# Performance work log

Hardware: AMD Instinct MI355X
Metric: run time of the kernel (lower is better)

Reference implementation:

```python
import jax, jax.numpy as jnp
import numpy as np

EPS = float(np.finfo(np.float32).eps)

# (joint_id, joint_name, parent_name) in the module's fkm_computation_order
ORDER = [
    (1, 'rHip', 'hip'), (2, 'rKnee', 'rHip'), (3, 'rAnkle', 'rKnee'), (4, 'rToe', 'rAnkle'),
    (6, 'lHip', 'hip'), (7, 'lKnee', 'lHip'), (8, 'lAnkle', 'lKnee'), (9, 'lToe', 'lAnkle'),
    (11, 'spine', 'hip'), (12, 'spine1', 'spine'), (13, 'thorax', 'spine1'), (14, 'neck', 'thorax'),
    (15, 'head', 'neck'), (16, 'lShoulderAnchor', 'spine1'), (17, 'lShoulder', 'lShoulderAnchor'),
    (18, 'lElbow', 'lShoulder'), (19, 'lWrist', 'lElbow'), (20, 'lThumb', 'lWrist'),
    (22, 'lWristEnd', 'lWrist'), (24, 'rShoulderAnchor', 'spine1'), (25, 'rShoulder', 'rShoulderAnchor'),
    (26, 'rElbow', 'rShoulder'), (27, 'rWrist', 'rElbow'), (28, 'rThumb', 'rWrist'),
    (30, 'rWristEnd', 'rWrist'),
]


def axis_angle_to_matrix(a):
    """Rodrigues formula, batched. a: [B,3] -> [B,3,3]."""
    theta = jnp.linalg.norm(a, axis=-1, keepdims=True)  # [B,1]
    r = a / (theta + EPS)                               # [B,3]
    r0, r1, r2 = r[:, 0], r[:, 1], r[:, 2]
    z = jnp.zeros_like(r0)
    # skew-symmetric S with S[0,1]=-r2, S[0,2]=r1, S[1,2]=-r0 (as in torch code)
    S = jnp.stack([
        jnp.stack([z, -r2, r1], axis=-1),
        jnp.stack([r2, z, -r0], axis=-1),
        jnp.stack([-r1, r0, z], axis=-1),
    ], axis=-2)  # [B,3,3]
    th = theta[..., None]  # [B,1,1]
    I = jnp.eye(3, dtype=a.dtype)
    return I + jnp.sin(th) * S + (1.0 - jnp.cos(th)) * (S @ S)


def setup_inputs() -> dict:
    key = jax.random.key(0)
    k1, k2 = jax.random.split(key)
    B = 262144
    x = jax.random.normal(k1, (B, 99), dtype=jnp.float32)
    offset = jax.random.normal(k2, (32, 3), dtype=jnp.float32)
    return {"x": x, "offset": offset}


def reference(x, offset):
    # hip root: position from first 3 dims, orientation from dims 3:6
    pos = {"hip": offset[0] + x[:, 0:3]}                # [B,3]
    ang = {"hip": axis_angle_to_matrix(x[:, 3:6])}      # [B,3,3]
    # local rotations for every joint in the chain: dims [3*id+3 : 3*id+6]
    local = {name: axis_angle_to_matrix(x[:, 3 * i + 3: 3 * i + 6]) for i, name, _ in ORDER}
    # sequential forward kinematics down the tree
    for i, cur, par in ORDER:
        # offset[i] @ R_parent  (row-vector times matrix), then translate
        pos[cur] = jnp.einsum('j,bjk->bk', offset[i], ang[par]) + pos[par]
        ang[cur] = local[cur] @ ang[par]
    # positions in the same order as get_joint_positions(): hip then chain order
    return jnp.stack([pos['hip']] + [pos[c] for _, c, _ in ORDER], axis=1)  # [B,26,3]
```

## Files before the change

### kernel.cpp

```cpp
#include <hip/hip_runtime.h>

#define ROWS 64
#define TPB  192
#define XDIM 99
#define NJ   26
#define OUTW 78

__device__ __forceinline__ float fast_rcp(float a)  { return __builtin_amdgcn_rcpf(a); }
__device__ __forceinline__ float fast_sqrt(float a) { return __builtin_amdgcn_sqrtf(a); }

__device__ __forceinline__ void rodrigues(float ax, float ay, float az, float* R) {
    const float EPS = 1.1920928955078125e-07f;
    float t = fast_sqrt(ax*ax + ay*ay + az*az);
    float inv = fast_rcp(t + EPS);
    float r0 = ax*inv, r1 = ay*inv, r2 = az*inv;
    float s = __sinf(t);
    float c = __cosf(t);
    float omc = 1.0f - c;
    float r00 = r0*r0, r11 = r1*r1, r22 = r2*r2;
    float r01 = r0*r1, r02 = r0*r2, r12 = r1*r2;
    R[0] = 1.0f - omc*(r11 + r22);
    R[1] = -s*r2 + omc*r01;
    R[2] =  s*r1 + omc*r02;
    R[3] =  s*r2 + omc*r01;
    R[4] = 1.0f - omc*(r00 + r22);
    R[5] = -s*r0 + omc*r12;
    R[6] = -s*r1 + omc*r02;
    R[7] =  s*r0 + omc*r12;
    R[8] = 1.0f - omc*(r00 + r11);
}

__global__ __launch_bounds__(TPB, 8) void skel_fk(const float* __restrict__ x,
                                                  const float* __restrict__ off,
                                                  float* __restrict__ out) {
    __shared__ float buf[ROWS * XDIM];
    const int t = threadIdx.x;
    const int w = t >> 6;
    const int l = t & 63;
    const int row0 = blockIdx.x * ROWS;

    {
        const float* gsrc = x + (long long)row0 * XDIM;
        const float* gw = gsrc + w * 2112 + l * 4;
        float* lw = buf + w * 2112;
        #pragma unroll
        for (int j = 0; j < 8; ++j) {
            __builtin_amdgcn_global_load_lds(
                (const __attribute__((address_space(1))) unsigned int*)(gw + j * 256),
                (__attribute__((address_space(3))) unsigned int*)(lw + j * 256),
                16, 0, 0);
        }
        __builtin_amdgcn_global_load_lds(
            (const __attribute__((address_space(1))) unsigned int*)(gsrc + w * 2112 + 2048 + l),
            (__attribute__((address_space(3))) unsigned int*)(buf + w * 2112 + 2048),
            4, 0, 0);
    }
    __syncthreads();

    const int r = l;
    const int k = w;
    float* wrow = &buf[r * XDIM];
    const float* row = wrow;

    constexpr int OFF_IDX[NJ] = {0,1,2,3,4,6,7,8,9,11,12,13,14,15,16,17,18,19,20,22,24,25,26,27,28,30};
    constexpr int PAR[NJ]     = {-1,0,1,2,3,0,5,6,7,0,9,10,11,12,10,14,15,16,17,17,10,20,21,22,23,23};

    float ac[NJ][3];
    float pp[NJ];

    {
        float R[9];
        rodrigues(row[3], row[4], row[5], R);
        ac[0][0] = (k == 0) ? R[0] : ((k == 1) ? R[1] : R[2]);
        ac[0][1] = (k == 0) ? R[3] : ((k == 1) ? R[4] : R[5]);
        ac[0][2] = (k == 0) ? R[6] : ((k == 1) ? R[7] : R[8]);
        pp[0] = off[k] + row[k];
    }

    #pragma unroll
    for (int s = 1; s < NJ; ++s) {
        const int i  = OFF_IDX[s];
        const int pa = PAR[s];
        float L[9];
        rodrigues(row[3*i+3], row[3*i+4], row[3*i+5], L);
        const float o0 = off[3*i], o1 = off[3*i+1], o2 = off[3*i+2];
        pp[s] = o0*ac[pa][0] + o1*ac[pa][1] + o2*ac[pa][2] + pp[pa];
        ac[s][0] = L[0]*ac[pa][0] + L[1]*ac[pa][1] + L[2]*ac[pa][2];
        ac[s][1] = L[3]*ac[pa][0] + L[4]*ac[pa][1] + L[5]*ac[pa][2];
        ac[s][2] = L[6]*ac[pa][0] + L[7]*ac[pa][1] + L[8]*ac[pa][2];
    }

    __syncthreads();

    #pragma unroll
    for (int s = 0; s < NJ; ++s)
        wrow[3*s + k] = pp[s];
    __syncthreads();

    {
        float* oblk = out + (long long)row0 * OUTW;
        #pragma unroll
        for (int j = 0; j < 26; ++j) {
            int m = t + j * TPB;
            int rr = m / OUTW;
            int cc = m - rr * OUTW;
            oblk[m] = buf[rr * XDIM + cc];
        }
    }
}

extern "C" void kernel_launch(void* const* d_in, const int* in_sizes, int n_in,
                              void* d_out, int out_size, void* d_ws, size_t ws_size,
                              hipStream_t stream) {
    const float* x   = (const float*)d_in[0];
    const float* off = (const float*)d_in[1];
    float* out = (float*)d_out;
    const int B = in_sizes[0] / XDIM;
    const int grid = B / ROWS;
    skel_fk<<<grid, TPB, 0, stream>>>(x, off, out);
}
```

Baseline: 40.11 us.

## Process two row slabs per block with both loads issued up front

Each block now handles two 64-row slabs. It issues the global-to-LDS loads for both slabs before the first barrier, then computes and writes each slab in turn. The barriers become lightweight lgkmcnt waits, sin and cos are fused into one sincos call, and launch bounds drop to 4 waves per SIMD. The aim is to amortize block launch and barrier overhead and to overlap the second slab's load with work. The cost is double the LDS per block, which halves occupancy.

```diff
diff --git a/kernel.cpp b/kernel.cpp
--- a/kernel.cpp
+++ b/kernel.cpp
@@ -1,10 +1,14 @@
 #include <hip/hip_runtime.h>
 
 #define ROWS 64
+#define NSLAB 2
 #define TPB  192
 #define XDIM 99
 #define NJ   26
 #define OUTW 78
+#define SLABF (ROWS * XDIM)
+
+#define LGKM_BAR() asm volatile("s_waitcnt lgkmcnt(0)\n\ts_barrier" ::: "memory")
 
 __device__ __forceinline__ float fast_rcp(float a)  { return __builtin_amdgcn_rcpf(a); }
 __device__ __forceinline__ float fast_sqrt(float a) { return __builtin_amdgcn_sqrtf(a); }
@@ -14,8 +18,8 @@
     float t = fast_sqrt(ax*ax + ay*ay + az*az);
     float inv = fast_rcp(t + EPS);
     float r0 = ax*inv, r1 = ay*inv, r2 = az*inv;
-    float s = __sinf(t);
-    float c = __cosf(t);
+    float s, c;
+    __sincosf(t, &s, &c);
     float omc = 1.0f - c;
     float r00 = r0*r0, r11 = r1*r1, r22 = r2*r2;
     float r01 = r0*r1, r02 = r0*r2, r12 = r1*r2;
@@ -30,19 +34,20 @@
     R[8] = 1.0f - omc*(r00 + r11);
 }
 
-__global__ __launch_bounds__(TPB, 8) void skel_fk(const float* __restrict__ x,
+__global__ __launch_bounds__(TPB, 4) void skel_fk(const float* __restrict__ x,
                                                   const float* __restrict__ off,
                                                   float* __restrict__ out) {
-    __shared__ float buf[ROWS * XDIM];
+    __shared__ float buf[NSLAB][SLABF];
     const int t = threadIdx.x;
     const int w = t >> 6;
     const int l = t & 63;
-    const int row0 = blockIdx.x * ROWS;
+    const int row0 = blockIdx.x * (ROWS * NSLAB);
 
-    {
-        const float* gsrc = x + (long long)row0 * XDIM;
-        const float* gw = gsrc + w * 2112 + l * 4;
-        float* lw = buf + w * 2112;
+    #pragma unroll
+    for (int sl = 0; sl < NSLAB; ++sl) {
+        const float* gs = x + (long long)(row0 + sl * ROWS) * XDIM;
+        const float* gw = gs + w * 2112 + l * 4;
+        float* lw = &buf[sl][0] + w * 2112;
         #pragma unroll
         for (int j = 0; j < 8; ++j) {
             __builtin_amdgcn_global_load_lds(
@@ -51,60 +56,63 @@
                 16, 0, 0);
         }
         __builtin_amdgcn_global_load_lds(
-            (const __attribute__((address_space(1))) unsigned int*)(gsrc + w * 2112 + 2048 + l),
-            (__attribute__((address_space(3))) unsigned int*)(buf + w * 2112 + 2048),
+            (const __attribute__((address_space(1))) unsigned int*)(gs + w * 2112 + 2048 + l),
+            (__attribute__((address_space(3))) unsigned int*)(&buf[sl][0] + w * 2112 + 2048),
             4, 0, 0);
     }
     __syncthreads();
 
-    const int r = l;
-    const int k = w;
-    float* wrow = &buf[r * XDIM];
-    const float* row = wrow;
-
     constexpr int OFF_IDX[NJ] = {0,1,2,3,4,6,7,8,9,11,12,13,14,15,16,17,18,19,20,22,24,25,26,27,28,30};
     constexpr int PAR[NJ]     = {-1,0,1,2,3,0,5,6,7,0,9,10,11,12,10,14,15,16,17,17,10,20,21,22,23,23};
 
-    float ac[NJ][3];
-    float pp[NJ];
-
-    {
-        float R[9];
-        rodrigues(row[3], row[4], row[5], R);
-        ac[0][0] = (k == 0) ? R[0] : ((k == 1) ? R[1] : R[2]);
-        ac[0][1] = (k == 0) ? R[3] : ((k == 1) ? R[4] : R[5]);
-        ac[0][2] = (k == 0) ? R[6] : ((k == 1) ? R[7] : R[8]);
-        pp[0] = off[k] + row[k];
-    }
+    const int k = w;
 
     #pragma unroll
-    for (int s = 1; s < NJ; ++s) {
-        const int i  = OFF_IDX[s];
-        const int pa = PAR[s];
-        float L[9];
-        rodrigues(row[3*i+3], row[3*i+4], row[3*i+5], L);
-        const float o0 = off[3*i], o1 = off[3*i+1], o2 = off[3*i+2];
-        pp[s] = o0*ac[pa][0] + o1*ac[pa][1] + o2*ac[pa][2] + pp[pa];
-        ac[s][0] = L[0]*ac[pa][0] + L[1]*ac[pa][1] + L[2]*ac[pa][2];
-        ac[s][1] = L[3]*ac[pa][0] + L[4]*ac[pa][1] + L[5]*ac[pa][2];
-        ac[s][2] = L[6]*ac[pa][0] + L[7]*ac[pa][1] + L[8]*ac[pa][2];
-    }
+    for (int sl = 0; sl < NSLAB; ++sl) {
+        float* wrow = &buf[sl][l * XDIM];
+        const float* row = wrow;
 
-    __syncthreads();
+        float ac[NJ][3];
+        float pp[NJ];
+        {
+            float R[9];
+            rodrigues(row[3], row[4], row[5], R);
+            ac[0][0] = (k == 0) ? R[0] : ((k == 1) ? R[1] : R[2]);
+            ac[0][1] = (k == 0) ? R[3] : ((k == 1) ? R[4] : R[5]);
+            ac[0][2] = (k == 0) ? R[6] : ((k == 1) ? R[7] : R[8]);
+            pp[0] = off[k] + row[k];
+        }
 
-    #pragma unroll
-    for (int s = 0; s < NJ; ++s)
-        wrow[3*s + k] = pp[s];
-    __syncthreads();
+        #pragma unroll
+        for (int s = 1; s < NJ; ++s) {
+            const int i  = OFF_IDX[s];
+            const int pa = PAR[s];
+            float L[9];
+            rodrigues(row[3*i+3], row[3*i+4], row[3*i+5], L);
+            const float o0 = off[3*i], o1 = off[3*i+1], o2 = off[3*i+2];
+            pp[s] = o0*ac[pa][0] + o1*ac[pa][1] + o2*ac[pa][2] + pp[pa];
+            ac[s][0] = L[0]*ac[pa][0] + L[1]*ac[pa][1] + L[2]*ac[pa][2];
+            ac[s][1] = L[3]*ac[pa][0] + L[4]*ac[pa][1] + L[5]*ac[pa][2];
+            ac[s][2] = L[6]*ac[pa][0] + L[7]*ac[pa][1] + L[8]*ac[pa][2];
+        }
 
-    {
-        float* oblk = out + (long long)row0 * OUTW;
+        LGKM_BAR();
+
         #pragma unroll
-        for (int j = 0; j < 26; ++j) {
-            int m = t + j * TPB;
-            int rr = m / OUTW;
-            int cc = m - rr * OUTW;
-            oblk[m] = buf[rr * XDIM + cc];
+        for (int s = 0; s < NJ; ++s)
+            wrow[3*s + k] = pp[s];
+
+        LGKM_BAR();
+
+        {
+            float* oblk = out + (long long)(row0 + sl * ROWS) * OUTW;
+            #pragma unroll
+            for (int j = 0; j < 26; ++j) {
+                int m = t + j * TPB;
+                int rr = m / OUTW;
+                int cc = m - rr * OUTW;
+                oblk[m] = buf[sl][rr * XDIM + cc];
+            }
         }
     }
 }
@@ -116,6 +124,6 @@
     const float* off = (const float*)d_in[1];
     float* out = (float*)d_out;
     const int B = in_sizes[0] / XDIM;
-    const int grid = B / ROWS;
+    const int grid = B / (ROWS * NSLAB);
     skel_fk<<<grid, TPB, 0, stream>>>(x, off, out);
 }
```

After: 43.19 us. 7.7% more time.
